# Optimization experiments

Hardware: AMD Instinct MI355X
Metric: run time of the kernel (lower is better)

Reference implementation:

```python
import jax, jax.numpy as jnp
import numpy as np

B, H, D = 32, 64, 128          # batch (decode), indexer heads, head dim
PAGE, PAGES = 64, 128          # cache page size, pages per sequence
S = PAGE * PAGES               # max kv len = 8192
NUM_PAGES = B * PAGES          # 4096 pages total
TOPK = 2048
SCALE = float(D) ** -0.5
FILL = -1


def setup_inputs() -> dict:
    key = jax.random.key(0)
    ks = jax.random.split(key, 6)
    q = jax.random.normal(ks[0], (B, H, D), dtype=jnp.float32)
    k = jax.random.normal(ks[1], (B, D), dtype=jnp.float32)          # current-step key
    weights = jax.random.uniform(ks[2], (B, H), dtype=jnp.float32)   # per-head gates
    # fp8 cache emulated as quantized values (k_cache) x per-token scales (k_s_cache)
    k_cache = jax.random.normal(ks[3], (NUM_PAGES, PAGE, D), dtype=jnp.float32)
    k_s_cache = jax.random.uniform(ks[4], (NUM_PAGES, PAGE), minval=0.5, maxval=1.5, dtype=jnp.float32)
    kv_seqlens = jax.random.randint(ks[5], (B,), S // 2, S + 1, dtype=jnp.int32)
    block_offsets = jnp.arange(NUM_PAGES, dtype=jnp.int32).reshape(B, PAGES)
    return dict(q=q, k=k, weights=weights, k_cache=k_cache, k_s_cache=k_s_cache,
                kv_seqlens=kv_seqlens, block_offsets=block_offsets)


def reference(q, k, weights, k_cache, k_s_cache, kv_seqlens, block_offsets):
    # Gather paged cache per sequence and dequantize: [B, S, D]
    kv = k_cache[block_offsets].reshape(B, S, D) * k_s_cache[block_offsets].reshape(B, S, 1)
    pos = jnp.arange(S, dtype=jnp.int32)
    # Current step's key lives at position kv_len - 1
    cur = pos[None, :] == (kv_seqlens[:, None] - 1)
    kv = jnp.where(cur[..., None], k[:, None, :], kv)
    # Indexer score: sum_h w[b,h] * relu(q[b,h] . k[b,s]) * scale
    logits = jnp.einsum('bhd,bsd->bhs', q, kv) * SCALE
    scores = jnp.einsum('bh,bhs->bs', weights, jax.nn.relu(logits))  # [B, S]
    valid = pos[None, :] < kv_seqlens[:, None]
    scores = jnp.where(valid, scores, -jnp.inf)
    vals, idx = jax.lax.top_k(scores, TOPK)
    idx = jnp.where(jnp.isfinite(vals), idx, FILL).astype(jnp.int32)
    return idx, scores
```

## Files before the change

### kernel.cpp

```cpp
#include <hip/hip_runtime.h>
#include <math.h>

#define NB 32
#define NH 64
#define ND 128
#define PAGE_SZ 64
#define NPAGES 128
#define NS 8192
#define NTOPK 2048
#define QSCALE 0.08838834764831845f
#define NEG_SENTINEL -3.0e38f

typedef __attribute__((ext_vector_type(8))) short short8;
typedef __attribute__((ext_vector_type(4))) float f32x4;

static __device__ __forceinline__ unsigned short f2bf(float x) {
    unsigned u = __float_as_uint(x);
    return (unsigned short)((u + 0x7FFFu + ((u >> 16) & 1u)) >> 16);
}

static __device__ __forceinline__ short8 pack8(const float4 &a, const float4 &b) {
    short8 r;
    r[0] = (short)f2bf(a.x); r[1] = (short)f2bf(a.y);
    r[2] = (short)f2bf(a.z); r[3] = (short)f2bf(a.w);
    r[4] = (short)f2bf(b.x); r[5] = (short)f2bf(b.y);
    r[6] = (short)f2bf(b.z); r[7] = (short)f2bf(b.w);
    return r;
}

__global__ __launch_bounds__(256) void score_kernel(
    const float* __restrict__ q,
    const float* __restrict__ kcur,
    const float* __restrict__ w,
    const float* __restrict__ kc,
    const float* __restrict__ ksc,
    const int*   __restrict__ kvlen,
    const int*   __restrict__ bo,
    float* __restrict__ scores_out)
{
    __shared__ __align__(16) unsigned short q_lds[64 * 128];
    __shared__ float w_lds[NH];

    const int b    = blockIdx.y;
    const int sb   = blockIdx.x;
    const int t    = threadIdx.x;
    const int wv   = t >> 6;
    const int lane = t & 63;
    const int len  = kvlen[b];
    const int cur  = len - 1;

    const float* qb = q + (size_t)b * NH * ND;
#pragma unroll
    for (int i = 0; i < 8; ++i) {
        int f = t + 256 * i;
        int row = f >> 5, d4 = f & 31;
        float4 v = *(const float4*)(qb + row * ND + d4 * 4);
        unsigned lo = f2bf(v.x) | ((unsigned)f2bf(v.y) << 16);
        unsigned hi = f2bf(v.z) | ((unsigned)f2bf(v.w) << 16);
        int ck = (d4 >> 1) ^ (row & 7);
        *(uint2*)(q_lds + row * 128 + (ck << 3) + (d4 & 1) * 4) = make_uint2(lo, hi);
    }
    if (t < NH) w_lds[t] = w[b * NH + t];
    __syncthreads();

    short8 aF[4][4];
#pragma unroll
    for (int hb = 0; hb < 4; ++hb)
#pragma unroll
        for (int ks = 0; ks < 4; ++ks) {
            int row = hb * 16 + (lane & 15);
            int ck = (ks * 4 + (lane >> 4)) ^ (row & 7);
            aF[hb][ks] = *(const short8*)(q_lds + row * 128 + (ck << 3));
        }
    float wgt[4][4];
#pragma unroll
    for (int hb = 0; hb < 4; ++hb)
#pragma unroll
        for (int r = 0; r < 4; ++r)
            wgt[hb][r] = w_lds[hb * 16 + (lane >> 4) * 4 + r];

    const int tok = wv * 16 + (lane & 15);
    const int l4  = lane >> 4;

    float4 gA[8], gB[8];
    float  scA, scB;

#define LOADP(P, G, SC)                                                       \
    {                                                                         \
        int pg = bo[b * NPAGES + sb * 4 + (P)];                               \
        int tg = sb * 256 + (P) * 64 + tok;                                   \
        bool iscur = (tg == cur);                                             \
        const float* kb = iscur ? (kcur + (size_t)b * ND)                     \
                                : (kc + (size_t)pg * (PAGE_SZ * ND) +         \
                                   (size_t)tok * ND);                         \
        SC = iscur ? 1.0f : ksc[pg * PAGE_SZ + tok];                          \
        _Pragma("unroll")                                                     \
        for (int ki = 0; ki < 4; ++ki) {                                      \
            G[2 * ki]     = *(const float4*)(kb + ki * 32 + l4 * 8);          \
            G[2 * ki + 1] = *(const float4*)(kb + ki * 32 + l4 * 8 + 4);      \
        }                                                                     \
    }

    LOADP(0, gA, scA)
#pragma unroll
    for (int p = 0; p < 4; ++p) {
        if (p < 3) LOADP(p + 1, gB, scB)

        short8 bF[4];
#pragma unroll
        for (int ki = 0; ki < 4; ++ki) bF[ki] = pack8(gA[2 * ki], gA[2 * ki + 1]);

        f32x4 acc[4];
#pragma unroll
        for (int hb = 0; hb < 4; ++hb) acc[hb] = (f32x4){0.f, 0.f, 0.f, 0.f};
#pragma unroll
        for (int ki = 0; ki < 4; ++ki)
#pragma unroll
            for (int hb = 0; hb < 4; ++hb)
                acc[hb] = __builtin_amdgcn_mfma_f32_16x16x32_bf16(
                    aF[hb][ki], bF[ki], acc[hb], 0, 0, 0);

        const float f = scA * QSCALE;
        float part = 0.f;
#pragma unroll
        for (int hb = 0; hb < 4; ++hb)
#pragma unroll
            for (int r = 0; r < 4; ++r)
                part += wgt[hb][r] * fmaxf(acc[hb][r] * f, 0.f);
        part += __shfl_xor(part, 16);
        part += __shfl_xor(part, 32);
        int sg = sb * 256 + p * 64 + tok;
        if (l4 == 0)
            scores_out[(size_t)b * NS + sg] = (sg < len) ? part : NEG_SENTINEL;

        if (p < 3) {
#pragma unroll
            for (int i = 0; i < 8; ++i) gA[i] = gB[i];
            scA = scB;
        }
    }
#undef LOADP
}

static __device__ __forceinline__ void cex(unsigned &a, unsigned &b, bool desc) {
    unsigned lo = a < b ? a : b;
    unsigned hi = a < b ? b : a;
    a = desc ? hi : lo;
    b = desc ? lo : hi;
}

__global__ __launch_bounds__(256) void topk_sort(
    const float* __restrict__ scores,
    unsigned* __restrict__ wsk)
{
    __shared__ unsigned keys[2048];
    const int b = blockIdx.y, c = blockIdx.x, t = threadIdx.x;
    const float* srow = scores + (size_t)b * NS + c * 2048;

    unsigned v[8];
    {
        float4 f0 = *(const float4*)(srow + t * 8);
        float4 f1 = *(const float4*)(srow + t * 8 + 4);
        float fv[8] = {f0.x, f0.y, f0.z, f0.w, f1.x, f1.y, f1.z, f1.w};
#pragma unroll
        for (int r = 0; r < 8; ++r) {
            int s = c * 2048 + t * 8 + r;
            float x = fv[r];
            v[r] = (x >= 0.f)
                 ? ((__float_as_uint(x) & 0xFFFFC000u) | (unsigned)(8192 - s))
                 : 0u;
        }
    }

    cex(v[0], v[1], true);  cex(v[2], v[3], false);
    cex(v[4], v[5], true);  cex(v[6], v[7], false);
    cex(v[0], v[2], true);  cex(v[1], v[3], true);
    cex(v[4], v[6], false); cex(v[5], v[7], false);
    cex(v[0], v[1], true);  cex(v[2], v[3], true);
    cex(v[4], v[5], false); cex(v[6], v[7], false);

    for (int k = 8; k <= 2048; k <<= 1) {
        const bool desc = (((unsigned)(t << 3)) & (unsigned)k) == 0u;
        for (int j = k >> 1; j >= 8; j >>= 1) {
            const int m = j >> 3;
            const bool keepHi = (((t & m) == 0) == desc);
            if (m < 64) {
#pragma unroll
                for (int r = 0; r < 8; ++r) {
                    unsigned o = __shfl_xor(v[r], m);
                    unsigned lo = v[r] < o ? v[r] : o;
                    unsigned hi = v[r] < o ? o : v[r];
                    v[r] = keepHi ? hi : lo;
                }
            } else {
                __syncthreads();
#pragma unroll
                for (int r = 0; r < 8; ++r) keys[t * 8 + r] = v[r];
                __syncthreads();
                const int pt = t ^ m;
#pragma unroll
                for (int r = 0; r < 8; ++r) {
                    unsigned o = keys[pt * 8 + r];
                    unsigned lo = v[r] < o ? v[r] : o;
                    unsigned hi = v[r] < o ? o : v[r];
                    v[r] = keepHi ? hi : lo;
                }
            }
        }
        cex(v[0], v[4], desc); cex(v[1], v[5], desc);
        cex(v[2], v[6], desc); cex(v[3], v[7], desc);
        cex(v[0], v[2], desc); cex(v[1], v[3], desc);
        cex(v[4], v[6], desc); cex(v[5], v[7], desc);
        cex(v[0], v[1], desc); cex(v[2], v[3], desc);
        cex(v[4], v[5], desc); cex(v[6], v[7], desc);
    }

    unsigned* wrow = wsk + ((size_t)b * 4 + c) * 2048;
#pragma unroll
    for (int r = 0; r < 8; ++r) wrow[t * 8 + r] = v[r];
}

__global__ __launch_bounds__(512) void topk_merge(
    const unsigned* __restrict__ wsk,
    int* __restrict__ idx_out)
{
    __shared__ unsigned keys[4096];
    const int b = blockIdx.x, t = threadIdx.x;
    const int g = t >> 8, tl = t & 255;
    const unsigned* base = wsk + (size_t)b * 4 * 2048;

    const unsigned* A = base + (2 * g) * 2048;
    const unsigned* B = base + (2 * g + 1) * 2048;
    unsigned v[8];
#pragma unroll
    for (int r = 0; r < 8; ++r) {
        int i = tl * 8 + r;
        unsigned a = A[i], bb = B[2047 - i];
        v[r] = a > bb ? a : bb;
    }
#pragma unroll
    for (int j = 1024; j >= 512; j >>= 1) {
        const int m = j >> 3;
        const bool keepHi = ((tl & m) == 0);
        __syncthreads();
#pragma unroll
        for (int r = 0; r < 8; ++r) keys[g * 2048 + tl * 8 + r] = v[r];
        __syncthreads();
        const int pt = tl ^ m;
#pragma unroll
        for (int r = 0; r < 8; ++r) {
            unsigned o = keys[g * 2048 + pt * 8 + r];
            unsigned lo = v[r] < o ? v[r] : o;
            unsigned hi = v[r] < o ? o : v[r];
            v[r] = keepHi ? hi : lo;
        }
    }
#pragma unroll
    for (int j = 256; j >= 8; j >>= 1) {
        const int m = j >> 3;
        const bool keepHi = ((tl & m) == 0);
#pragma unroll
        for (int r = 0; r < 8; ++r) {
            unsigned o = __shfl_xor(v[r], m);
            unsigned lo = v[r] < o ? v[r] : o;
            unsigned hi = v[r] < o ? o : v[r];
            v[r] = keepHi ? hi : lo;
        }
    }
    cex(v[0], v[4], true); cex(v[1], v[5], true);
    cex(v[2], v[6], true); cex(v[3], v[7], true);
    cex(v[0], v[2], true); cex(v[1], v[3], true);
    cex(v[4], v[6], true); cex(v[5], v[7], true);
    cex(v[0], v[1], true); cex(v[2], v[3], true);
    cex(v[4], v[5], true); cex(v[6], v[7], true);

    __syncthreads();
#pragma unroll
    for (int r = 0; r < 8; ++r) keys[g * 2048 + tl * 8 + r] = v[r];
    __syncthreads();

    unsigned u[4];
#pragma unroll
    for (int r = 0; r < 4; ++r) {
        int i = t * 4 + r;
        unsigned a = keys[i], bb = keys[2048 + 2047 - i];
        u[r] = a > bb ? a : bb;
    }
#pragma unroll
    for (int j = 1024; j >= 256; j >>= 1) {
        const int m = j >> 2;
        const bool keepHi = ((t & m) == 0);
        __syncthreads();
#pragma unroll
        for (int r = 0; r < 4; ++r) keys[t * 4 + r] = u[r];
        __syncthreads();
        const int pt = t ^ m;
#pragma unroll
        for (int r = 0; r < 4; ++r) {
            unsigned o = keys[pt * 4 + r];
            unsigned lo = u[r] < o ? u[r] : o;
            unsigned hi = u[r] < o ? o : u[r];
            u[r] = keepHi ? hi : lo;
        }
    }
#pragma unroll
    for (int j = 128; j >= 4; j >>= 1) {
        const int m = j >> 2;
        const bool keepHi = ((t & m) == 0);
#pragma unroll
        for (int r = 0; r < 4; ++r) {
            unsigned o = __shfl_xor(u[r], m);
            unsigned lo = u[r] < o ? u[r] : o;
            unsigned hi = u[r] < o ? o : u[r];
            u[r] = keepHi ? hi : lo;
        }
    }
    cex(u[0], u[2], true); cex(u[1], u[3], true);
    cex(u[0], u[1], true); cex(u[2], u[3], true);

#pragma unroll
    for (int r = 0; r < 4; ++r) {
        unsigned key = u[r];
        idx_out[b * NTOPK + t * 4 + r] =
            key ? (int)(8192u - (key & 0x3FFFu)) : -1;
    }
}

extern "C" void kernel_launch(void* const* d_in, const int* in_sizes, int n_in,
                              void* d_out, int out_size, void* d_ws, size_t ws_size,
                              hipStream_t stream)
{
    const float* q     = (const float*)d_in[0];
    const float* kcur  = (const float*)d_in[1];
    const float* w     = (const float*)d_in[2];
    const float* kc    = (const float*)d_in[3];
    const float* ksc   = (const float*)d_in[4];
    const int*   kvlen = (const int*)d_in[5];
    const int*   bo    = (const int*)d_in[6];

    int*      idx_out    = (int*)d_out;
    float*    scores_out = (float*)d_out + (size_t)NB * NTOPK;
    unsigned* wsk        = (unsigned*)d_ws;

    score_kernel<<<dim3(32, NB), 256, 0, stream>>>(q, kcur, w, kc, ksc, kvlen,
                                                   bo, scores_out);
    topk_sort<<<dim3(4, NB), 256, 0, stream>>>(scores_out, wsk);
    topk_merge<<<NB, 512, 0, stream>>>(wsk, idx_out);
}
```

Before: 48.16 us.

## Fuse top-k sort and merge into one 1024-thread kernel; use packed bf16 conversion

Merges the per-chunk bitonic sort and the two-stage merge into one kernel per batch row with 1024 threads and an 8192-entry shared key array. This removes the workspace round trip and one launch. It also swaps the manual bf16 rounding for the packed __float22bfloat162_rn intrinsic, and moves the per-token scale out of the relu/weight loop into a single multiply before the store. The trade-off is that only 32 blocks run the sort, which lowers parallelism during the sort phase, and the block needs 32KB of LDS.

Result: slower. 51.68 us (+7.3%).

```diff
diff --git a/kernel.cpp b/kernel.cpp
--- a/kernel.cpp
+++ b/kernel.cpp
@@ -1,4 +1,5 @@
 #include <hip/hip_runtime.h>
+#include <hip/hip_bf16.h>
 #include <math.h>
 
 #define NB 32
@@ -14,18 +15,19 @@
 typedef __attribute__((ext_vector_type(8))) short short8;
 typedef __attribute__((ext_vector_type(4))) float f32x4;
 
-static __device__ __forceinline__ unsigned short f2bf(float x) {
-    unsigned u = __float_as_uint(x);
-    return (unsigned short)((u + 0x7FFFu + ((u >> 16) & 1u)) >> 16);
+static __device__ __forceinline__ unsigned pack2(float x, float y) {
+    union { __hip_bfloat162 h; unsigned u; } c;
+    c.h = __float22bfloat162_rn(make_float2(x, y));
+    return c.u;
 }
 
 static __device__ __forceinline__ short8 pack8(const float4 &a, const float4 &b) {
-    short8 r;
-    r[0] = (short)f2bf(a.x); r[1] = (short)f2bf(a.y);
-    r[2] = (short)f2bf(a.z); r[3] = (short)f2bf(a.w);
-    r[4] = (short)f2bf(b.x); r[5] = (short)f2bf(b.y);
-    r[6] = (short)f2bf(b.z); r[7] = (short)f2bf(b.w);
-    return r;
+    union { unsigned u[4]; short8 s; } c;
+    c.u[0] = pack2(a.x, a.y);
+    c.u[1] = pack2(a.z, a.w);
+    c.u[2] = pack2(b.x, b.y);
+    c.u[3] = pack2(b.z, b.w);
+    return c.s;
 }
 
 __global__ __launch_bounds__(256) void score_kernel(
@@ -55,8 +57,8 @@
         int f = t + 256 * i;
         int row = f >> 5, d4 = f & 31;
         float4 v = *(const float4*)(qb + row * ND + d4 * 4);
-        unsigned lo = f2bf(v.x) | ((unsigned)f2bf(v.y) << 16);
-        unsigned hi = f2bf(v.z) | ((unsigned)f2bf(v.w) << 16);
+        unsigned lo = pack2(v.x, v.y);
+        unsigned hi = pack2(v.z, v.w);
         int ck = (d4 >> 1) ^ (row & 7);
         *(uint2*)(q_lds + row * 128 + (ck << 3) + (d4 & 1) * 4) = make_uint2(lo, hi);
     }
@@ -120,18 +122,19 @@
                 acc[hb] = __builtin_amdgcn_mfma_f32_16x16x32_bf16(
                     aF[hb][ki], bF[ki], acc[hb], 0, 0, 0);
 
-        const float f = scA * QSCALE;
         float part = 0.f;
 #pragma unroll
         for (int hb = 0; hb < 4; ++hb)
 #pragma unroll
             for (int r = 0; r < 4; ++r)
-                part += wgt[hb][r] * fmaxf(acc[hb][r] * f, 0.f);
+                part = fmaf(wgt[hb][r], fmaxf(acc[hb][r], 0.f), part);
         part += __shfl_xor(part, 16);
         part += __shfl_xor(part, 32);
         int sg = sb * 256 + p * 64 + tok;
-        if (l4 == 0)
-            scores_out[(size_t)b * NS + sg] = (sg < len) ? part : NEG_SENTINEL;
+        if (l4 == 0) {
+            float val = part * (scA * QSCALE);
+            scores_out[(size_t)b * NS + sg] = (sg < len) ? val : NEG_SENTINEL;
+        }
 
         if (p < 3) {
 #pragma unroll
@@ -149,22 +152,23 @@
     b = desc ? lo : hi;
 }
 
-__global__ __launch_bounds__(256) void topk_sort(
+__global__ __launch_bounds__(1024) void topk_kernel(
     const float* __restrict__ scores,
-    unsigned* __restrict__ wsk)
+    int* __restrict__ idx_out)
 {
-    __shared__ unsigned keys[2048];
-    const int b = blockIdx.y, c = blockIdx.x, t = threadIdx.x;
-    const float* srow = scores + (size_t)b * NS + c * 2048;
-
+    __shared__ unsigned keys[NS];
+    const int b = blockIdx.x, t = threadIdx.x;
+    const int g = t >> 8, tl = t & 255;
+
+    const float* srow = scores + (size_t)b * NS + g * 2048;
     unsigned v[8];
     {
-        float4 f0 = *(const float4*)(srow + t * 8);
-        float4 f1 = *(const float4*)(srow + t * 8 + 4);
+        float4 f0 = *(const float4*)(srow + tl * 8);
+        float4 f1 = *(const float4*)(srow + tl * 8 + 4);
         float fv[8] = {f0.x, f0.y, f0.z, f0.w, f1.x, f1.y, f1.z, f1.w};
 #pragma unroll
         for (int r = 0; r < 8; ++r) {
-            int s = c * 2048 + t * 8 + r;
+            int s = g * 2048 + tl * 8 + r;
             float x = fv[r];
             v[r] = (x >= 0.f)
                  ? ((__float_as_uint(x) & 0xFFFFC000u) | (unsigned)(8192 - s))
@@ -180,10 +184,10 @@
     cex(v[4], v[5], false); cex(v[6], v[7], false);
 
     for (int k = 8; k <= 2048; k <<= 1) {
-        const bool desc = (((unsigned)(t << 3)) & (unsigned)k) == 0u;
+        const bool desc = (((unsigned)(tl << 3)) & (unsigned)k) == 0u;
         for (int j = k >> 1; j >= 8; j >>= 1) {
             const int m = j >> 3;
-            const bool keepHi = (((t & m) == 0) == desc);
+            const bool keepHi = (((tl & m) == 0) == desc);
             if (m < 64) {
 #pragma unroll
                 for (int r = 0; r < 8; ++r) {
@@ -195,12 +199,12 @@
             } else {
                 __syncthreads();
 #pragma unroll
-                for (int r = 0; r < 8; ++r) keys[t * 8 + r] = v[r];
+                for (int r = 0; r < 8; ++r) keys[g * 2048 + tl * 8 + r] = v[r];
                 __syncthreads();
-                const int pt = t ^ m;
+                const int pt = tl ^ m;
 #pragma unroll
                 for (int r = 0; r < 8; ++r) {
-                    unsigned o = keys[pt * 8 + r];
+                    unsigned o = keys[g * 2048 + pt * 8 + r];
                     unsigned lo = v[r] < o ? v[r] : o;
                     unsigned hi = v[r] < o ? o : v[r];
                     v[r] = keepHi ? hi : lo;
@@ -215,114 +219,105 @@
         cex(v[4], v[5], desc); cex(v[6], v[7], desc);
     }
 
-    unsigned* wrow = wsk + ((size_t)b * 4 + c) * 2048;
-#pragma unroll
-    for (int r = 0; r < 8; ++r) wrow[t * 8 + r] = v[r];
-}
-
-__global__ __launch_bounds__(512) void topk_merge(
-    const unsigned* __restrict__ wsk,
-    int* __restrict__ idx_out)
-{
-    __shared__ unsigned keys[4096];
-    const int b = blockIdx.x, t = threadIdx.x;
-    const int g = t >> 8, tl = t & 255;
-    const unsigned* base = wsk + (size_t)b * 4 * 2048;
-
-    const unsigned* A = base + (2 * g) * 2048;
-    const unsigned* B = base + (2 * g + 1) * 2048;
-    unsigned v[8];
-#pragma unroll
-    for (int r = 0; r < 8; ++r) {
-        int i = tl * 8 + r;
-        unsigned a = A[i], bb = B[2047 - i];
-        v[r] = a > bb ? a : bb;
-    }
-#pragma unroll
-    for (int j = 1024; j >= 512; j >>= 1) {
-        const int m = j >> 3;
-        const bool keepHi = ((tl & m) == 0);
-        __syncthreads();
-#pragma unroll
-        for (int r = 0; r < 8; ++r) keys[g * 2048 + tl * 8 + r] = v[r];
-        __syncthreads();
-        const int pt = tl ^ m;
-#pragma unroll
-        for (int r = 0; r < 8; ++r) {
-            unsigned o = keys[g * 2048 + pt * 8 + r];
-            unsigned lo = v[r] < o ? v[r] : o;
-            unsigned hi = v[r] < o ? o : v[r];
-            v[r] = keepHi ? hi : lo;
-        }
-    }
-#pragma unroll
-    for (int j = 256; j >= 8; j >>= 1) {
-        const int m = j >> 3;
-        const bool keepHi = ((tl & m) == 0);
-#pragma unroll
-        for (int r = 0; r < 8; ++r) {
-            unsigned o = __shfl_xor(v[r], m);
-            unsigned lo = v[r] < o ? v[r] : o;
-            unsigned hi = v[r] < o ? o : v[r];
-            v[r] = keepHi ? hi : lo;
-        }
-    }
-    cex(v[0], v[4], true); cex(v[1], v[5], true);
-    cex(v[2], v[6], true); cex(v[3], v[7], true);
-    cex(v[0], v[2], true); cex(v[1], v[3], true);
-    cex(v[4], v[6], true); cex(v[5], v[7], true);
-    cex(v[0], v[1], true); cex(v[2], v[3], true);
-    cex(v[4], v[5], true); cex(v[6], v[7], true);
-
     __syncthreads();
 #pragma unroll
     for (int r = 0; r < 8; ++r) keys[g * 2048 + tl * 8 + r] = v[r];
     __syncthreads();
 
-    unsigned u[4];
-#pragma unroll
-    for (int r = 0; r < 4; ++r) {
-        int i = t * 4 + r;
-        unsigned a = keys[i], bb = keys[2048 + 2047 - i];
-        u[r] = a > bb ? a : bb;
-    }
-#pragma unroll
-    for (int j = 1024; j >= 256; j >>= 1) {
-        const int m = j >> 2;
-        const bool keepHi = ((t & m) == 0);
+    {
+        const int p = t >> 9, tp = t & 511;
+        unsigned u[4];
+#pragma unroll
+        for (int r = 0; r < 4; ++r) {
+            int i = tp * 4 + r;
+            unsigned a = keys[p * 4096 + i];
+            unsigned c = keys[p * 4096 + 2048 + (2047 - i)];
+            u[r] = a > c ? a : c;
+        }
+#pragma unroll
+        for (int j = 1024; j >= 256; j >>= 1) {
+            const int m = j >> 2;
+            const bool keepHi = ((tp & m) == 0);
+            __syncthreads();
+#pragma unroll
+            for (int r = 0; r < 4; ++r) keys[t * 4 + r] = u[r];
+            __syncthreads();
+            const int pt = t ^ m;
+#pragma unroll
+            for (int r = 0; r < 4; ++r) {
+                unsigned o = keys[pt * 4 + r];
+                unsigned lo = u[r] < o ? u[r] : o;
+                unsigned hi = u[r] < o ? o : u[r];
+                u[r] = keepHi ? hi : lo;
+            }
+        }
+#pragma unroll
+        for (int j = 128; j >= 4; j >>= 1) {
+            const int m = j >> 2;
+            const bool keepHi = ((tp & m) == 0);
+#pragma unroll
+            for (int r = 0; r < 4; ++r) {
+                unsigned o = __shfl_xor(u[r], m);
+                unsigned lo = u[r] < o ? u[r] : o;
+                unsigned hi = u[r] < o ? o : u[r];
+                u[r] = keepHi ? hi : lo;
+            }
+        }
+        cex(u[0], u[2], true); cex(u[1], u[3], true);
+        cex(u[0], u[1], true); cex(u[2], u[3], true);
+
         __syncthreads();
 #pragma unroll
         for (int r = 0; r < 4; ++r) keys[t * 4 + r] = u[r];
         __syncthreads();
-        const int pt = t ^ m;
-#pragma unroll
-        for (int r = 0; r < 4; ++r) {
-            unsigned o = keys[pt * 4 + r];
-            unsigned lo = u[r] < o ? u[r] : o;
-            unsigned hi = u[r] < o ? o : u[r];
-            u[r] = keepHi ? hi : lo;
-        }
-    }
-#pragma unroll
-    for (int j = 128; j >= 4; j >>= 1) {
-        const int m = j >> 2;
-        const bool keepHi = ((t & m) == 0);
-#pragma unroll
-        for (int r = 0; r < 4; ++r) {
-            unsigned o = __shfl_xor(u[r], m);
-            unsigned lo = u[r] < o ? u[r] : o;
-            unsigned hi = u[r] < o ? o : u[r];
-            u[r] = keepHi ? hi : lo;
-        }
-    }
-    cex(u[0], u[2], true); cex(u[1], u[3], true);
-    cex(u[0], u[1], true); cex(u[2], u[3], true);
-
-#pragma unroll
-    for (int r = 0; r < 4; ++r) {
-        unsigned key = u[r];
-        idx_out[b * NTOPK + t * 4 + r] =
-            key ? (int)(8192u - (key & 0x3FFFu)) : -1;
+    }
+
+    {
+        unsigned u[2];
+#pragma unroll
+        for (int r = 0; r < 2; ++r) {
+            int i = t * 2 + r;
+            unsigned a = keys[i];
+            unsigned c = keys[2048 + (2047 - i)];
+            u[r] = a > c ? a : c;
+        }
+#pragma unroll
+        for (int j = 1024; j >= 128; j >>= 1) {
+            const int m = j >> 1;
+            const bool keepHi = ((t & m) == 0);
+            __syncthreads();
+#pragma unroll
+            for (int r = 0; r < 2; ++r) keys[t * 2 + r] = u[r];
+            __syncthreads();
+            const int pt = t ^ m;
+#pragma unroll
+            for (int r = 0; r < 2; ++r) {
+                unsigned o = keys[pt * 2 + r];
+                unsigned lo = u[r] < o ? u[r] : o;
+                unsigned hi = u[r] < o ? o : u[r];
+                u[r] = keepHi ? hi : lo;
+            }
+        }
+#pragma unroll
+        for (int j = 64; j >= 2; j >>= 1) {
+            const int m = j >> 1;
+            const bool keepHi = ((t & m) == 0);
+#pragma unroll
+            for (int r = 0; r < 2; ++r) {
+                unsigned o = __shfl_xor(u[r], m);
+                unsigned lo = u[r] < o ? u[r] : o;
+                unsigned hi = u[r] < o ? o : u[r];
+                u[r] = keepHi ? hi : lo;
+            }
+        }
+        cex(u[0], u[1], true);
+
+#pragma unroll
+        for (int r = 0; r < 2; ++r) {
+            unsigned key = u[r];
+            idx_out[b * NTOPK + t * 2 + r] =
+                key ? (int)(8192u - (key & 0x3FFFu)) : -1;
+        }
     }
 }
 
@@ -338,12 +333,10 @@
     const int*   kvlen = (const int*)d_in[5];
     const int*   bo    = (const int*)d_in[6];
 
-    int*      idx_out    = (int*)d_out;
-    float*    scores_out = (float*)d_out + (size_t)NB * NTOPK;
-    unsigned* wsk        = (unsigned*)d_ws;
+    int*   idx_out    = (int*)d_out;
+    float* scores_out = (float*)d_out + (size_t)NB * NTOPK;
 
     score_kernel<<<dim3(32, NB), 256, 0, stream>>>(q, kcur, w, kc, ksc, kvlen,
                                                    bo, scores_out);
-    topk_sort<<<dim3(4, NB), 256, 0, stream>>>(scores_out, wsk);
-    topk_merge<<<NB, 512, 0, stream>>>(wsk, idx_out);
-}
+    topk_kernel<<<NB, 1024, 0, stream>>>(scores_out, idx_out);
+}
```

## Issue first K page load before Q staging and single-buffer K prefetch

Applied to the files above, without the earlier changes.

Moves the first page's K cache load ahead of the Q bf16 conversion and LDS staging so global latency overlaps that setup. The double-buffered gA/gB registers become a single buffer that is reloaded right after packing to bf16, which cuts register pressure, and a launch bound of 3 blocks per CU is requested. The per-token scale multiply is also factored out of the relu sum and applied once after the reduction, which is valid because the scale is positive. The risk is that the compiler-enforced occupancy target could cause spills.

Result: no change. 48.57 us (+0.9%).

```diff
diff --git a/kernel.cpp b/kernel.cpp
--- a/kernel.cpp
+++ b/kernel.cpp
@@ -28,7 +28,7 @@
     return r;
 }
 
-__global__ __launch_bounds__(256) void score_kernel(
+__global__ __launch_bounds__(256, 3) void score_kernel(
     const float* __restrict__ q,
     const float* __restrict__ kcur,
     const float* __restrict__ w,
@@ -49,6 +49,30 @@
     const int len  = kvlen[b];
     const int cur  = len - 1;
 
+    const int tok = wv * 16 + (lane & 15);
+    const int l4  = lane >> 4;
+
+    float4 gA[8];
+    float  scA;
+
+#define LOADP(P)                                                              \
+    {                                                                         \
+        int pg = bo[b * NPAGES + sb * 4 + (P)];                               \
+        int tg = sb * 256 + (P) * 64 + tok;                                   \
+        bool iscur = (tg == cur);                                             \
+        const float* kb = iscur ? (kcur + (size_t)b * ND)                     \
+                                : (kc + (size_t)pg * (PAGE_SZ * ND) +         \
+                                   (size_t)tok * ND);                         \
+        scA = iscur ? 1.0f : ksc[pg * PAGE_SZ + tok];                         \
+        _Pragma("unroll")                                                     \
+        for (int ki = 0; ki < 4; ++ki) {                                      \
+            gA[2 * ki]     = *(const float4*)(kb + ki * 32 + l4 * 8);         \
+            gA[2 * ki + 1] = *(const float4*)(kb + ki * 32 + l4 * 8 + 4);     \
+        }                                                                     \
+    }
+
+    LOADP(0)
+
     const float* qb = q + (size_t)b * NH * ND;
 #pragma unroll
     for (int i = 0; i < 8; ++i) {
@@ -79,36 +103,14 @@
         for (int r = 0; r < 4; ++r)
             wgt[hb][r] = w_lds[hb * 16 + (lane >> 4) * 4 + r];
 
-    const int tok = wv * 16 + (lane & 15);
-    const int l4  = lane >> 4;
-
-    float4 gA[8], gB[8];
-    float  scA, scB;
-
-#define LOADP(P, G, SC)                                                       \
-    {                                                                         \
-        int pg = bo[b * NPAGES + sb * 4 + (P)];                               \
-        int tg = sb * 256 + (P) * 64 + tok;                                   \
-        bool iscur = (tg == cur);                                             \
-        const float* kb = iscur ? (kcur + (size_t)b * ND)                     \
-                                : (kc + (size_t)pg * (PAGE_SZ * ND) +         \
-                                   (size_t)tok * ND);                         \
-        SC = iscur ? 1.0f : ksc[pg * PAGE_SZ + tok];                          \
-        _Pragma("unroll")                                                     \
-        for (int ki = 0; ki < 4; ++ki) {                                      \
-            G[2 * ki]     = *(const float4*)(kb + ki * 32 + l4 * 8);          \
-            G[2 * ki + 1] = *(const float4*)(kb + ki * 32 + l4 * 8 + 4);      \
-        }                                                                     \
-    }
-
-    LOADP(0, gA, scA)
 #pragma unroll
     for (int p = 0; p < 4; ++p) {
-        if (p < 3) LOADP(p + 1, gB, scB)
-
         short8 bF[4];
 #pragma unroll
         for (int ki = 0; ki < 4; ++ki) bF[ki] = pack8(gA[2 * ki], gA[2 * ki + 1]);
+        const float scP = scA;
+
+        if (p < 3) LOADP(p + 1)
 
         f32x4 acc[4];
 #pragma unroll
@@ -120,23 +122,18 @@
                 acc[hb] = __builtin_amdgcn_mfma_f32_16x16x32_bf16(
                     aF[hb][ki], bF[ki], acc[hb], 0, 0, 0);
 
-        const float f = scA * QSCALE;
         float part = 0.f;
 #pragma unroll
         for (int hb = 0; hb < 4; ++hb)
 #pragma unroll
             for (int r = 0; r < 4; ++r)
-                part += wgt[hb][r] * fmaxf(acc[hb][r] * f, 0.f);
+                part = fmaf(wgt[hb][r], fmaxf(acc[hb][r], 0.f), part);
         part += __shfl_xor(part, 16);
         part += __shfl_xor(part, 32);
         int sg = sb * 256 + p * 64 + tok;
-        if (l4 == 0)
-            scores_out[(size_t)b * NS + sg] = (sg < len) ? part : NEG_SENTINEL;
-
-        if (p < 3) {
-#pragma unroll
-            for (int i = 0; i < 8; ++i) gA[i] = gB[i];
-            scA = scB;
+        if (l4 == 0) {
+            float val = part * (scP * QSCALE);
+            scores_out[(size_t)b * NS + sg] = (sg < len) ? val : NEG_SENTINEL;
         }
     }
 #undef LOADP
```
